# Optimization experiments

Measured on AMD Instinct MI355X. Metric: run time of the kernel, lower is better.

Reference implementation:

```python
import jax, jax.numpy as jnp
import numpy as np

N = 50000
E = 800000
D_IN, D_HID, D_OUT = 128, 128, 64
BN_EPS = 1e-5

def _glorot(key, shape):
    fan_in = shape[-1]
    return jax.random.normal(key, shape, dtype=jnp.float32) / jnp.sqrt(jnp.float32(fan_in))

def setup_inputs() -> dict:
    key = jax.random.key(0)
    ks = jax.random.split(key, 16)
    x = jax.random.normal(ks[0], (N, D_IN), dtype=jnp.float32)
    edge_index = jax.random.randint(ks[1], (2, E), 0, N, dtype=jnp.int64)
    edge_pairs = jax.random.randint(ks[2], (2, E), 0, N, dtype=jnp.int64)
    return {
        "x": x,
        "edge_index": edge_index,
        "edge_pairs": edge_pairs,
        # SAGEConv1: lin_l (bias) on aggregated neighbors, lin_r (no bias) on root
        "c1_Wl": _glorot(ks[3], (D_HID, D_IN)),
        "c1_bl": jnp.zeros((D_HID,), jnp.float32),
        "c1_Wr": _glorot(ks[4], (D_HID, D_IN)),
        # BatchNorm1d (eval mode: running stats)
        "bn_gamma": jnp.ones((D_HID,), jnp.float32),
        "bn_beta": jnp.zeros((D_HID,), jnp.float32),
        "bn_mean": jnp.zeros((D_HID,), jnp.float32),
        "bn_var": jnp.ones((D_HID,), jnp.float32),
        # SAGEConv2
        "c2_Wl": _glorot(ks[5], (D_OUT, D_HID)),
        "c2_bl": jnp.zeros((D_OUT,), jnp.float32),
        "c2_Wr": _glorot(ks[6], (D_OUT, D_HID)),
        # EdgeRegHead MLP: Linear(2*D_OUT, D_OUT) -> ReLU -> Linear(D_OUT, D_OUT//2) -> ReLU -> Linear(D_OUT//2, 1) -> Sigmoid
        "e_W1": _glorot(ks[7], (D_OUT, 2 * D_OUT)),
        "e_b1": jnp.zeros((D_OUT,), jnp.float32),
        "e_W2": _glorot(ks[8], (D_OUT // 2, D_OUT)),
        "e_b2": jnp.zeros((D_OUT // 2,), jnp.float32),
        "e_W3": _glorot(ks[9], (1, D_OUT // 2)),
        "e_b3": jnp.zeros((1,), jnp.float32),
    }

def _sage_conv(x, src, dst, Wl, bl, Wr):
    # mean-aggregate source features at destination nodes (PyG SAGEConv mean aggr)
    msg_sum = jax.ops.segment_sum(x[src], dst, num_segments=N)          # [N, d]
    cnt = jax.ops.segment_sum(jnp.ones((src.shape[0],), x.dtype), dst, num_segments=N)
    mean = msg_sum / jnp.maximum(cnt, 1.0)[:, None]
    return mean @ Wl.T + bl + x @ Wr.T

def reference(x, edge_index, edge_pairs,
              c1_Wl, c1_bl, c1_Wr,
              bn_gamma, bn_beta, bn_mean, bn_var,
              c2_Wl, c2_bl, c2_Wr,
              e_W1, e_b1, e_W2, e_b2, e_W3, e_b3):
    src, dst = edge_index[0], edge_index[1]
    h = _sage_conv(x, src, dst, c1_Wl, c1_bl, c1_Wr)                    # [N, D_HID]
    h = (h - bn_mean) * jax.lax.rsqrt(bn_var + BN_EPS) * bn_gamma + bn_beta
    h = jax.nn.relu(h)                                                   # dropout inactive (eval)
    z = _sage_conv(h, src, dst, c2_Wl, c2_bl, c2_Wr)                    # [N, D_OUT]
    zi = z[edge_pairs[0]]                                               # [P, D_OUT]
    zj = z[edge_pairs[1]]
    e = jnp.concatenate([zi, zj], axis=-1)                              # [P, 2*D_OUT]
    e = jax.nn.relu(e @ e_W1.T + e_b1)
    e = jax.nn.relu(e @ e_W2.T + e_b2)
    return jax.nn.sigmoid(e @ e_W3.T + e_b3)                            # [P, 1]
```

## Files before the change

### kernel.cpp

```cpp
#include <hip/hip_runtime.h>
#include <hip/hip_bf16.h>
#include <math.h>

#define NN 50000
#define NE 800000
#define DIN 128
#define DHID 128
#define DOUT 64
#define BN_EPS 1e-5f

typedef __attribute__((ext_vector_type(8))) short bf16x8;
typedef __attribute__((ext_vector_type(8))) _Float16 f16x8;
typedef __attribute__((ext_vector_type(4))) _Float16 f16x4;
typedef __attribute__((ext_vector_type(2))) _Float16 f16x2;
typedef __attribute__((ext_vector_type(4))) float f32x4;
typedef unsigned short ushort_t;
typedef unsigned int uint_t;

__device__ __forceinline__ ushort_t f2bf(float f) {
    uint_t u = __float_as_uint(f);
    uint_t r = (u + 0x7FFFu + ((u >> 16) & 1u)) >> 16;
    return (ushort_t)r;
}

__device__ __forceinline__ uint_t pk2bf(float a, float b) {
    __hip_bfloat16 x = __float2bfloat16(a);
    __hip_bfloat16 y = __float2bfloat16(b);
    ushort_t ux = *reinterpret_cast<ushort_t*>(&x);
    ushort_t uy = *reinterpret_cast<ushort_t*>(&y);
    return (uint_t)ux | ((uint_t)uy << 16);
}

__global__ __launch_bounds__(256) void k_deg_xcast(
    const int* __restrict__ ei, int* __restrict__ deg,
    const float* __restrict__ x, _Float16* __restrict__ xh)
{
    int b = blockIdx.x;
    if (b < 3125) {
        int e = b * 256 + threadIdx.x;
        atomicAdd(deg + ei[NE + e], 1);
    } else {
        int i = (b - 3125) * 256 + threadIdx.x;
        const float4* src = (const float4*)x + (size_t)i * 2;
        float4 a = src[0], c = src[1];
        f16x8 o;
        o[0] = (_Float16)a.x; o[1] = (_Float16)a.y; o[2] = (_Float16)a.z; o[3] = (_Float16)a.w;
        o[4] = (_Float16)c.x; o[5] = (_Float16)c.y; o[6] = (_Float16)c.z; o[7] = (_Float16)c.w;
        *(f16x8*)(xh + (size_t)i * 8) = o;
    }
}

__global__ __launch_bounds__(256) void k_scan1_prep(
    const int* __restrict__ deg, int* __restrict__ part,
    const float* __restrict__ c1_Wl, const float* __restrict__ c1_Wr,
    const float* __restrict__ c2_Wl, const float* __restrict__ c2_Wr,
    const float* __restrict__ gam, const float* __restrict__ bet,
    const float* __restrict__ bmean, const float* __restrict__ bvar,
    const float* __restrict__ eW1, const float* __restrict__ eW2,
    _Float16* __restrict__ w1cat, _Float16* __restrict__ w2cat,
    ushort_t* __restrict__ w1bf, ushort_t* __restrict__ w2bf,
    float* __restrict__ bnsc, float* __restrict__ bnsh)
{
    int t = threadIdx.x;
    if (blockIdx.x < 49) {
        __shared__ int s[256];
        int g = blockIdx.x * 256 + t;
        int v = 0;
        if (g < 12500) { int4 d = ((const int4*)deg)[g]; v = d.x + d.y + d.z + d.w; }
        s[t] = v;
        __syncthreads();
        #pragma unroll
        for (int off = 128; off > 0; off >>= 1) {
            if (t < off) s[t] += s[t + off];
            __syncthreads();
        }
        if (t == 0) part[blockIdx.x] = s[0];
    } else {
        for (int i = t; i < 128 * 128; i += 256) {
            int row = i >> 7, k = i & 127;
            w1cat[row * 256 + k]       = (_Float16)c1_Wl[i];
            w1cat[row * 256 + 128 + k] = (_Float16)c1_Wr[i];
        }
        for (int i = t; i < 64 * 128; i += 256) {
            int row = i >> 7, k = i & 127;
            w2cat[row * 256 + k]       = (_Float16)c2_Wl[i];
            w2cat[row * 256 + 128 + k] = (_Float16)c2_Wr[i];
        }
        for (int i = t; i < 64 * 128; i += 256) w1bf[i] = f2bf(eW1[i]);
        for (int i = t; i < 32 * 64; i += 256)  w2bf[i] = f2bf(eW2[i]);
        for (int i = t; i < 128; i += 256) {
            float s = gam[i] * rsqrtf(bvar[i] + BN_EPS);
            bnsc[i] = s;
            bnsh[i] = bet[i] - bmean[i] * s;
        }
    }
}

__global__ __launch_bounds__(256) void k_scan3(
    const int* __restrict__ deg, const int* __restrict__ part, int* __restrict__ rowptr)
{
    __shared__ int s[256];
    __shared__ int p[64];
    int t = threadIdx.x;
    int b = blockIdx.x;
    int g = b * 256 + t;
    int4 d = make_int4(0, 0, 0, 0);
    if (g < 12500) d = ((const int4*)deg)[g];
    int sum4 = d.x + d.y + d.z + d.w;
    s[t] = sum4;
    if (t < 49) p[t] = part[t];
    __syncthreads();
    #pragma unroll
    for (int off = 1; off < 256; off <<= 1) {
        int v = (t >= off) ? s[t - off] : 0;
        __syncthreads();
        s[t] += v;
        __syncthreads();
    }
    int blockoff = 0;
    for (int i = 0; i < b; ++i) blockoff += p[i];
    int off0 = blockoff + s[t] - sum4;
    if (g < 12500) {
        int4 o;
        o.x = off0;
        o.y = off0 + d.x;
        o.z = o.y + d.y;
        o.w = o.z + d.z;
        ((int4*)rowptr)[g] = o;
        if (g == 12499) rowptr[NN] = o.w + d.w;
    }
}

__global__ __launch_bounds__(256) void k_fill(
    const int* __restrict__ ei, const int* __restrict__ rowptr,
    int* __restrict__ cursor, int* __restrict__ csr_src)
{
    int e = blockIdx.x * blockDim.x + threadIdx.x;
    if (e >= NE) return;
    int dst = ei[NE + e];
    int slot = atomicAdd(cursor + dst, 1);
    csr_src[rowptr[dst] + slot] = ei[e];
}

#define GATHER4(feat)                                                          \
    {                                                                          \
        _Pragma("unroll 1")                                                    \
        for (int q = 0; q < 4; ++q) {                                          \
            int n = w * 4 + q;                                                 \
            int node = tile * 16 + n;                                          \
            int beg = __builtin_amdgcn_readfirstlane(rowptr[node]);            \
            int end = __builtin_amdgcn_readfirstlane(rowptr[node + 1]);        \
            float2 a0 = {0.f,0.f}, a1 = {0.f,0.f}, a2 = {0.f,0.f}, a3 = {0.f,0.f}; \
            float2 a4 = {0.f,0.f}, a5 = {0.f,0.f}, a6 = {0.f,0.f}, a7 = {0.f,0.f}; \
            int j = beg;                                                       \
            for (; j + 7 < end; j += 8) {                                      \
                int s0 = csr_src[j];     int s1 = csr_src[j + 1];              \
                int s2 = csr_src[j + 2]; int s3 = csr_src[j + 3];              \
                int s4 = csr_src[j + 4]; int s5 = csr_src[j + 5];              \
                int s6 = csr_src[j + 6]; int s7 = csr_src[j + 7];              \
                f16x2 v0 = *(const f16x2*)(feat + (size_t)s0 * 128 + lane * 2);\
                f16x2 v1 = *(const f16x2*)(feat + (size_t)s1 * 128 + lane * 2);\
                f16x2 v2 = *(const f16x2*)(feat + (size_t)s2 * 128 + lane * 2);\
                f16x2 v3 = *(const f16x2*)(feat + (size_t)s3 * 128 + lane * 2);\
                f16x2 v4 = *(const f16x2*)(feat + (size_t)s4 * 128 + lane * 2);\
                f16x2 v5 = *(const f16x2*)(feat + (size_t)s5 * 128 + lane * 2);\
                f16x2 v6 = *(const f16x2*)(feat + (size_t)s6 * 128 + lane * 2);\
                f16x2 v7 = *(const f16x2*)(feat + (size_t)s7 * 128 + lane * 2);\
                a0.x += (float)v0[0]; a0.y += (float)v0[1];                    \
                a1.x += (float)v1[0]; a1.y += (float)v1[1];                    \
                a2.x += (float)v2[0]; a2.y += (float)v2[1];                    \
                a3.x += (float)v3[0]; a3.y += (float)v3[1];                    \
                a4.x += (float)v4[0]; a4.y += (float)v4[1];                    \
                a5.x += (float)v5[0]; a5.y += (float)v5[1];                    \
                a6.x += (float)v6[0]; a6.y += (float)v6[1];                    \
                a7.x += (float)v7[0]; a7.y += (float)v7[1];                    \
            }                                                                  \
            for (; j + 1 < end; j += 2) {                                      \
                int s0 = csr_src[j];                                           \
                int s1 = csr_src[j + 1];                                       \
                f16x2 v0 = *(const f16x2*)(feat + (size_t)s0 * 128 + lane * 2);\
                f16x2 v1 = *(const f16x2*)(feat + (size_t)s1 * 128 + lane * 2);\
                a0.x += (float)v0[0]; a0.y += (float)v0[1];                    \
                a1.x += (float)v1[0]; a1.y += (float)v1[1];                    \
            }                                                                  \
            if (j < end) {                                                     \
                int s0 = csr_src[j];                                           \
                f16x2 v0 = *(const f16x2*)(feat + (size_t)s0 * 128 + lane * 2);\
                a0.x += (float)v0[0]; a0.y += (float)v0[1];                    \
            }                                                                  \
            float inv = 1.0f / fmaxf((float)(end - beg), 1.0f);                \
            f16x2 o;                                                           \
            o[0] = (_Float16)((a0.x + a1.x + a2.x + a3.x + a4.x + a5.x + a6.x + a7.x) * inv); \
            o[1] = (_Float16)((a0.y + a1.y + a2.y + a3.y + a4.y + a5.y + a6.y + a7.y) * inv); \
            uint_t off = (uint_t)(n * 256 + lane * 4) ^ (uint_t)((n & 7) << 4);\
            *(f16x2*)((char*)mlds + off) = o;                                  \
        }                                                                      \
    }

__global__ __launch_bounds__(256) void k_gconv1(
    const _Float16* __restrict__ xh, const int* __restrict__ rowptr,
    const int* __restrict__ csr_src,
    const _Float16* __restrict__ w1cat, const float* __restrict__ bl,
    const float* __restrict__ bnsc, const float* __restrict__ bnsh,
    _Float16* __restrict__ hh)
{
    __shared__ _Float16 mlds[16 * 128];
    const int tid = threadIdx.x;
    const int lane = tid & 63;
    const int w = tid >> 6;
    const int tile = blockIdx.x;
    const int e = lane & 15;
    const int c = lane >> 4;
    const int node = tile * 16 + e;

    f16x8 wf[2][8];
    #pragma unroll
    for (int nt = 0; nt < 2; ++nt)
        #pragma unroll
        for (int ks = 0; ks < 8; ++ks)
            wf[nt][ks] = *(const f16x8*)(w1cat + (size_t)(w * 32 + nt * 16 + e) * 256 + ks * 32 + c * 8);
    f16x8 bfx[4];
    #pragma unroll
    for (int ks = 0; ks < 4; ++ks)
        bfx[ks] = *(const f16x8*)(xh + (size_t)node * 128 + ks * 32 + c * 8);
    f32x4 acc[2];
    #pragma unroll
    for (int nt = 0; nt < 2; ++nt)
        acc[nt] = *(const f32x4*)(bl + w * 32 + nt * 16 + c * 4);

    GATHER4(xh);
    __syncthreads();

    f16x8 bfm[4];
    #pragma unroll
    for (int ks = 0; ks < 4; ++ks) {
        uint_t off = (uint_t)(e * 256 + ks * 64 + c * 16) ^ (uint_t)((e & 7) << 4);
        bfm[ks] = *(const f16x8*)((const char*)mlds + off);
    }

    #pragma unroll
    for (int ks = 0; ks < 4; ++ks)
        #pragma unroll
        for (int nt = 0; nt < 2; ++nt)
            acc[nt] = __builtin_amdgcn_mfma_f32_16x16x32_f16(wf[nt][ks], bfm[ks], acc[nt], 0, 0, 0);
    #pragma unroll
    for (int ks = 0; ks < 4; ++ks)
        #pragma unroll
        for (int nt = 0; nt < 2; ++nt)
            acc[nt] = __builtin_amdgcn_mfma_f32_16x16x32_f16(wf[nt][ks + 4], bfx[ks], acc[nt], 0, 0, 0);

    #pragma unroll
    for (int nt = 0; nt < 2; ++nt) {
        int j0 = w * 32 + nt * 16 + c * 4;
        f32x4 sc = *(const f32x4*)(bnsc + j0);
        f32x4 sh = *(const f32x4*)(bnsh + j0);
        f16x4 o;
        #pragma unroll
        for (int r = 0; r < 4; ++r)
            o[r] = (_Float16)fmaxf(acc[nt][r] * sc[r] + sh[r], 0.f);
        *(f16x4*)(hh + (size_t)node * 128 + j0) = o;
    }
}

__global__ __launch_bounds__(256) void k_gconv2(
    const _Float16* __restrict__ hh, const int* __restrict__ rowptr,
    const int* __restrict__ csr_src,
    const _Float16* __restrict__ w2cat, const float* __restrict__ bl,
    ushort_t* __restrict__ zbf)
{
    __shared__ _Float16 mlds[16 * 128];
    const int tid = threadIdx.x;
    const int lane = tid & 63;
    const int w = tid >> 6;
    const int tile = blockIdx.x;
    const int e = lane & 15;
    const int c = lane >> 4;
    const int node = tile * 16 + e;

    f16x8 wf[8];
    #pragma unroll
    for (int ks = 0; ks < 8; ++ks)
        wf[ks] = *(const f16x8*)(w2cat + (size_t)(w * 16 + e) * 256 + ks * 32 + c * 8);
    f16x8 bfx[4];
    #pragma unroll
    for (int ks = 0; ks < 4; ++ks)
        bfx[ks] = *(const f16x8*)(hh + (size_t)node * 128 + ks * 32 + c * 8);
    f32x4 acc = *(const f32x4*)(bl + w * 16 + c * 4);

    GATHER4(hh);
    __syncthreads();

    f16x8 bfm[4];
    #pragma unroll
    for (int ks = 0; ks < 4; ++ks) {
        uint_t off = (uint_t)(e * 256 + ks * 64 + c * 16) ^ (uint_t)((e & 7) << 4);
        bfm[ks] = *(const f16x8*)((const char*)mlds + off);
    }

    #pragma unroll
    for (int ks = 0; ks < 4; ++ks)
        acc = __builtin_amdgcn_mfma_f32_16x16x32_f16(wf[ks], bfm[ks], acc, 0, 0, 0);
    #pragma unroll
    for (int ks = 0; ks < 4; ++ks)
        acc = __builtin_amdgcn_mfma_f32_16x16x32_f16(wf[ks + 4], bfx[ks], acc, 0, 0, 0);

    int j0 = w * 16 + c * 4;
    uint2 pk;
    pk.x = pk2bf(acc[0], acc[1]);
    pk.y = pk2bf(acc[2], acc[3]);
    *(uint2*)(zbf + (size_t)node * 64 + j0) = pk;
}

__global__ __launch_bounds__(256) void k_edge(
    const ushort_t* __restrict__ zbf, const int* __restrict__ ep,
    const ushort_t* __restrict__ w1bf, const float* __restrict__ b1,
    const ushort_t* __restrict__ w2bf, const float* __restrict__ b2,
    const float* __restrict__ W3, const float* __restrict__ b3,
    float* __restrict__ out)
{
    __shared__ ushort_t a1lds[4][16 * 64];
    const int tid  = threadIdx.x;
    const int lane = tid & 63;
    const int e    = lane & 15;
    const int c    = lane >> 4;
    ushort_t* lds  = &a1lds[tid >> 6][0];
    const uint_t swz = (uint_t)((e & 7) << 4);

    bf16x8 w1f[4][4];
    #pragma unroll
    for (int mt = 0; mt < 4; ++mt)
        #pragma unroll
        for (int ks = 0; ks < 4; ++ks)
            w1f[mt][ks] = *(const bf16x8*)(w1bf + (mt * 16 + e) * 128 + ks * 32 + c * 8);

    bf16x8 w2f[2][2];
    #pragma unroll
    for (int mt2 = 0; mt2 < 2; ++mt2)
        #pragma unroll
        for (int ks2 = 0; ks2 < 2; ++ks2)
            w2f[mt2][ks2] = *(const bf16x8*)(w2bf + (mt2 * 16 + e) * 64 + ks2 * 32 + c * 8);

    f32x4 bias1[4];
    #pragma unroll
    for (int mt = 0; mt < 4; ++mt) bias1[mt] = *(const f32x4*)(b1 + mt * 16 + c * 4);
    f32x4 bias2[2];
    #pragma unroll
    for (int mt2 = 0; mt2 < 2; ++mt2) bias2[mt2] = *(const f32x4*)(b2 + mt2 * 16 + c * 4);
    f32x4 w3v[2];
    #pragma unroll
    for (int mt2 = 0; mt2 < 2; ++mt2) w3v[mt2] = *(const f32x4*)(W3 + mt2 * 16 + c * 4);
    const float b3v = b3[0];

    const int nw = (gridDim.x * blockDim.x) >> 6;
    const int NT = NE / 16;

#define LOADZ(T, dst)                                                         \
    {                                                                         \
        int p = (T) * 16 + e;                                                 \
        int ni = ep[p];                                                       \
        int nj = ep[NE + p];                                                  \
        const ushort_t* zi = zbf + (size_t)ni * DOUT;                         \
        const ushort_t* zj = zbf + (size_t)nj * DOUT;                         \
        dst[0] = *(const bf16x8*)(zi + c * 8);                                \
        dst[1] = *(const bf16x8*)(zi + 32 + c * 8);                           \
        dst[2] = *(const bf16x8*)(zj + c * 8);                                \
        dst[3] = *(const bf16x8*)(zj + 32 + c * 8);                           \
    }

#define COMPUTE(T, bfr)                                                       \
    {                                                                         \
        f32x4 acc[4];                                                         \
        _Pragma("unroll")                                                     \
        for (int mt = 0; mt < 4; ++mt) acc[mt] = bias1[mt];                   \
        __builtin_amdgcn_s_setprio(1);                                        \
        _Pragma("unroll")                                                     \
        for (int ks = 0; ks < 4; ++ks)                                        \
            _Pragma("unroll")                                                 \
            for (int mt = 0; mt < 4; ++mt)                                    \
                acc[mt] = __builtin_amdgcn_mfma_f32_16x16x32_bf16(            \
                    w1f[mt][ks], bfr[ks], acc[mt], 0, 0, 0);                  \
        __builtin_amdgcn_s_setprio(0);                                        \
        _Pragma("unroll")                                                     \
        for (int mt = 0; mt < 4; ++mt) {                                      \
            uint_t lo = pk2bf(fmaxf(acc[mt][0], 0.f), fmaxf(acc[mt][1], 0.f));\
            uint_t hi = pk2bf(fmaxf(acc[mt][2], 0.f), fmaxf(acc[mt][3], 0.f));\
            uint_t off = (uint_t)(e * 128 + mt * 32 + c * 8) ^ swz;           \
            *(uint2*)((char*)lds + off) = make_uint2(lo, hi);                 \
        }                                                                     \
        bf16x8 b2f[2];                                                        \
        _Pragma("unroll")                                                     \
        for (int ks2 = 0; ks2 < 2; ++ks2) {                                   \
            uint_t off = (uint_t)(e * 128 + ks2 * 64 + c * 16) ^ swz;         \
            b2f[ks2] = *(const bf16x8*)((const char*)lds + off);              \
        }                                                                     \
        f32x4 a2[2];                                                          \
        _Pragma("unroll")                                                     \
        for (int mt2 = 0; mt2 < 2; ++mt2) a2[mt2] = bias2[mt2];               \
        __builtin_amdgcn_s_setprio(1);                                        \
        _Pragma("unroll")                                                     \
        for (int ks2 = 0; ks2 < 2; ++ks2)                                     \
            _Pragma("unroll")                                                 \
            for (int mt2 = 0; mt2 < 2; ++mt2)                                 \
                a2[mt2] = __builtin_amdgcn_mfma_f32_16x16x32_bf16(            \
                    w2f[mt2][ks2], b2f[ks2], a2[mt2], 0, 0, 0);               \
        __builtin_amdgcn_s_setprio(0);                                        \
        float t3 = b3v;                                                       \
        _Pragma("unroll")                                                     \
        for (int mt2 = 0; mt2 < 2; ++mt2)                                     \
            _Pragma("unroll")                                                 \
            for (int r = 0; r < 4; ++r)                                       \
                t3 += fmaxf(a2[mt2][r], 0.f) * w3v[mt2][r];                   \
        t3 += __shfl_xor(t3, 16);                                             \
        t3 += __shfl_xor(t3, 32);                                             \
        if (lane < 16) {                                                      \
            float ex = __expf(-t3);                                           \
            out[(T) * 16 + lane] = __builtin_amdgcn_rcpf(1.f + ex);           \
        }                                                                     \
    }

    bf16x8 zA[4], zB[4];
    int tile = (blockIdx.x * blockDim.x + tid) >> 6;
    if (tile >= NT) return;
    LOADZ(tile, zA);
    while (tile < NT) {
        int nx = tile + nw;
        if (nx < NT) LOADZ(nx, zB);
        COMPUTE(tile, zA);
        tile = nx;
        if (tile >= NT) break;
        nx = tile + nw;
        if (nx < NT) LOADZ(nx, zA);
        COMPUTE(tile, zB);
        tile = nx;
    }

#undef LOADZ
#undef COMPUTE
}

extern "C" void kernel_launch(void* const* d_in, const int* in_sizes, int n_in,
                              void* d_out, int out_size, void* d_ws, size_t ws_size,
                              hipStream_t stream)
{
    const float* x     = (const float*)d_in[0];
    const int*   ei    = (const int*)d_in[1];
    const int*   ep    = (const int*)d_in[2];
    const float* c1_Wl = (const float*)d_in[3];
    const float* c1_bl = (const float*)d_in[4];
    const float* c1_Wr = (const float*)d_in[5];
    const float* bn_g  = (const float*)d_in[6];
    const float* bn_b  = (const float*)d_in[7];
    const float* bn_m  = (const float*)d_in[8];
    const float* bn_v  = (const float*)d_in[9];
    const float* c2_Wl = (const float*)d_in[10];
    const float* c2_bl = (const float*)d_in[11];
    const float* c2_Wr = (const float*)d_in[12];
    const float* e_W1  = (const float*)d_in[13];
    const float* e_b1  = (const float*)d_in[14];
    const float* e_W2  = (const float*)d_in[15];
    const float* e_b2  = (const float*)d_in[16];
    const float* e_W3  = (const float*)d_in[17];
    const float* e_b3  = (const float*)d_in[18];
    float* out = (float*)d_out;

    _Float16* xh    = (_Float16*)d_ws;
    _Float16* meanh = xh + (size_t)NN * DIN;
    _Float16* hh    = meanh + (size_t)NN * DIN;
    ushort_t* zbf   = (ushort_t*)(hh + (size_t)NN * DHID);
    _Float16* w1cat = (_Float16*)(zbf + (size_t)NN * DOUT);
    _Float16* w2cat = w1cat + 128 * 256;
    ushort_t* w1bf  = (ushort_t*)(w2cat + 64 * 256);
    ushort_t* w2bf  = w1bf + 64 * 128;
    float*    bnsc  = (float*)(w2bf + 32 * 64);
    float*    bnsh  = bnsc + 128;
    int*      deg     = (int*)(bnsh + 128);
    int*      cursor  = deg + 50048;
    int*      rowptr  = cursor + 50048;
    int*      csr_src = rowptr + 50052;
    int*      part    = csr_src + 800000;

    hipMemsetAsync(deg, 0, (size_t)(50048 * 2) * sizeof(int), stream);

    k_deg_xcast<<<6250, 256, 0, stream>>>(ei, deg, x, xh);
    k_scan1_prep<<<50, 256, 0, stream>>>(deg, part,
                                         c1_Wl, c1_Wr, c2_Wl, c2_Wr,
                                         bn_g, bn_b, bn_m, bn_v, e_W1, e_W2,
                                         w1cat, w2cat, w1bf, w2bf, bnsc, bnsh);
    k_scan3<<<49, 256, 0, stream>>>(deg, part, rowptr);
    k_fill <<<3125, 256, 0, stream>>>(ei, rowptr, cursor, csr_src);

    k_gconv1<<<3125, 256, 0, stream>>>(xh, rowptr, csr_src, w1cat, c1_bl, bnsc, bnsh, hh);
    k_gconv2<<<3125, 256, 0, stream>>>(hh, rowptr, csr_src, w2cat, c2_bl, zbf);

    k_edge<<<1280, 256, 0, stream>>>(zbf, ep, w1bf, e_b1, w2bf, e_b2,
                                     e_W3, e_b3, out);
}
```

Baseline: 295.7 us.

## Project layer-2 features before aggregation to halve gather width

Adds a kernel that computes h·Wl^T (64-wide fp16) per node before aggregation, so the second conv gathers 64-wide projected rows instead of 128-wide hidden rows and then adds the mean to the root-term MFMA result. This uses linearity of mean aggregation to cut the gather traffic of layer 2 in half, at the cost of an extra kernel launch and an extra pass over hh. Also removes s_setprio hints in the edge MLP and changes the edge kernel grid size. Gathers are now per-lane scalar fp16 loads, which may be less efficient per byte.

```diff
diff --git a/kernel.cpp b/kernel.cpp
--- a/kernel.cpp
+++ b/kernel.cpp
@@ -142,14 +142,14 @@
     csr_src[rowptr[dst] + slot] = ei[e];
 }
 
-#define GATHER4(feat)                                                          \
+#define GATHER4_128(feat)                                                      \
     {                                                                          \
         _Pragma("unroll 1")                                                    \
         for (int q = 0; q < 4; ++q) {                                          \
             int n = w * 4 + q;                                                 \
-            int node = tile * 16 + n;                                          \
-            int beg = __builtin_amdgcn_readfirstlane(rowptr[node]);            \
-            int end = __builtin_amdgcn_readfirstlane(rowptr[node + 1]);        \
+            int node4 = tile * 16 + n;                                         \
+            int beg = __builtin_amdgcn_readfirstlane(rowptr[node4]);           \
+            int end = __builtin_amdgcn_readfirstlane(rowptr[node4 + 1]);       \
             float2 a0 = {0.f,0.f}, a1 = {0.f,0.f}, a2 = {0.f,0.f}, a3 = {0.f,0.f}; \
             float2 a4 = {0.f,0.f}, a5 = {0.f,0.f}, a6 = {0.f,0.f}, a7 = {0.f,0.f}; \
             int j = beg;                                                       \
@@ -228,7 +228,7 @@
     for (int nt = 0; nt < 2; ++nt)
         acc[nt] = *(const f32x4*)(bl + w * 32 + nt * 16 + c * 4);
 
-    GATHER4(xh);
+    GATHER4_128(xh);
     __syncthreads();
 
     f16x8 bfm[4];
@@ -262,13 +262,44 @@
     }
 }
 
+__global__ __launch_bounds__(256) void k_hw(
+    const _Float16* __restrict__ hh, const _Float16* __restrict__ w2cat,
+    _Float16* __restrict__ hw)
+{
+    const int tid = threadIdx.x;
+    const int lane = tid & 63;
+    const int e = lane & 15;
+    const int c = lane >> 4;
+    const int w = tid >> 6;
+    const int node = blockIdx.x * 16 + e;
+
+    f16x8 wf[4];
+    #pragma unroll
+    for (int ks = 0; ks < 4; ++ks)
+        wf[ks] = *(const f16x8*)(w2cat + (size_t)(w * 16 + e) * 256 + ks * 32 + c * 8);
+    f16x8 bf[4];
+    #pragma unroll
+    for (int ks = 0; ks < 4; ++ks)
+        bf[ks] = *(const f16x8*)(hh + (size_t)node * 128 + ks * 32 + c * 8);
+
+    f32x4 acc = {0.f, 0.f, 0.f, 0.f};
+    #pragma unroll
+    for (int ks = 0; ks < 4; ++ks)
+        acc = __builtin_amdgcn_mfma_f32_16x16x32_f16(wf[ks], bf[ks], acc, 0, 0, 0);
+
+    f16x4 o;
+    #pragma unroll
+    for (int r = 0; r < 4; ++r) o[r] = (_Float16)acc[r];
+    *(f16x4*)(hw + (size_t)node * 64 + w * 16 + c * 4) = o;
+}
+
 __global__ __launch_bounds__(256) void k_gconv2(
-    const _Float16* __restrict__ hh, const int* __restrict__ rowptr,
-    const int* __restrict__ csr_src,
+    const _Float16* __restrict__ hh, const _Float16* __restrict__ hw,
+    const int* __restrict__ rowptr, const int* __restrict__ csr_src,
     const _Float16* __restrict__ w2cat, const float* __restrict__ bl,
     ushort_t* __restrict__ zbf)
 {
-    __shared__ _Float16 mlds[16 * 128];
+    __shared__ float mlds32[16 * 64];
     const int tid = threadIdx.x;
     const int lane = tid & 63;
     const int w = tid >> 6;
@@ -277,32 +308,65 @@
     const int c = lane >> 4;
     const int node = tile * 16 + e;
 
-    f16x8 wf[8];
-    #pragma unroll
-    for (int ks = 0; ks < 8; ++ks)
-        wf[ks] = *(const f16x8*)(w2cat + (size_t)(w * 16 + e) * 256 + ks * 32 + c * 8);
+    f16x8 wf[4];
+    #pragma unroll
+    for (int ks = 0; ks < 4; ++ks)
+        wf[ks] = *(const f16x8*)(w2cat + (size_t)(w * 16 + e) * 256 + 128 + ks * 32 + c * 8);
     f16x8 bfx[4];
     #pragma unroll
     for (int ks = 0; ks < 4; ++ks)
         bfx[ks] = *(const f16x8*)(hh + (size_t)node * 128 + ks * 32 + c * 8);
+
+    #pragma unroll 1
+    for (int q = 0; q < 4; ++q) {
+        int n = w * 4 + q;
+        int node4 = tile * 16 + n;
+        int beg = __builtin_amdgcn_readfirstlane(rowptr[node4]);
+        int end = __builtin_amdgcn_readfirstlane(rowptr[node4 + 1]);
+        float a0 = 0.f, a1 = 0.f, a2 = 0.f, a3 = 0.f;
+        float a4 = 0.f, a5 = 0.f, a6 = 0.f, a7 = 0.f;
+        int j = beg;
+        for (; j + 7 < end; j += 8) {
+            int s0 = csr_src[j];     int s1 = csr_src[j + 1];
+            int s2 = csr_src[j + 2]; int s3 = csr_src[j + 3];
+            int s4 = csr_src[j + 4]; int s5 = csr_src[j + 5];
+            int s6 = csr_src[j + 6]; int s7 = csr_src[j + 7];
+            a0 += (float)hw[(size_t)s0 * 64 + lane];
+            a1 += (float)hw[(size_t)s1 * 64 + lane];
+            a2 += (float)hw[(size_t)s2 * 64 + lane];
+            a3 += (float)hw[(size_t)s3 * 64 + lane];
+            a4 += (float)hw[(size_t)s4 * 64 + lane];
+            a5 += (float)hw[(size_t)s5 * 64 + lane];
+            a6 += (float)hw[(size_t)s6 * 64 + lane];
+            a7 += (float)hw[(size_t)s7 * 64 + lane];
+        }
+        for (; j + 1 < end; j += 2) {
+            int s0 = csr_src[j];
+            int s1 = csr_src[j + 1];
+            a0 += (float)hw[(size_t)s0 * 64 + lane];
+            a1 += (float)hw[(size_t)s1 * 64 + lane];
+        }
+        if (j < end) {
+            int s0 = csr_src[j];
+            a0 += (float)hw[(size_t)s0 * 64 + lane];
+        }
+        float inv = 1.0f / fmaxf((float)(end - beg), 1.0f);
+        float m = (a0 + a1 + a2 + a3 + a4 + a5 + a6 + a7) * inv;
+        uint_t off = (uint_t)(n * 256 + lane * 4) ^ (uint_t)((n & 7) << 4);
+        *(float*)((char*)mlds32 + off) = m;
+    }
+    __syncthreads();
+
     f32x4 acc = *(const f32x4*)(bl + w * 16 + c * 4);
-
-    GATHER4(hh);
-    __syncthreads();
-
-    f16x8 bfm[4];
-    #pragma unroll
-    for (int ks = 0; ks < 4; ++ks) {
-        uint_t off = (uint_t)(e * 256 + ks * 64 + c * 16) ^ (uint_t)((e & 7) << 4);
-        bfm[ks] = *(const f16x8*)((const char*)mlds + off);
-    }
-
-    #pragma unroll
-    for (int ks = 0; ks < 4; ++ks)
-        acc = __builtin_amdgcn_mfma_f32_16x16x32_f16(wf[ks], bfm[ks], acc, 0, 0, 0);
-    #pragma unroll
-    for (int ks = 0; ks < 4; ++ks)
-        acc = __builtin_amdgcn_mfma_f32_16x16x32_f16(wf[ks + 4], bfx[ks], acc, 0, 0, 0);
+    {
+        uint_t off = (uint_t)(e * 256 + (w * 16 + c * 4) * 4) ^ (uint_t)((e & 7) << 4);
+        f32x4 mv = *(const f32x4*)((const char*)mlds32 + off);
+        acc[0] += mv[0]; acc[1] += mv[1]; acc[2] += mv[2]; acc[3] += mv[3];
+    }
+
+    #pragma unroll
+    for (int ks = 0; ks < 4; ++ks)
+        acc = __builtin_amdgcn_mfma_f32_16x16x32_f16(wf[ks], bfx[ks], acc, 0, 0, 0);
 
     int j0 = w * 16 + c * 4;
     uint2 pk;
@@ -372,14 +436,12 @@
         f32x4 acc[4];                                                         \
         _Pragma("unroll")                                                     \
         for (int mt = 0; mt < 4; ++mt) acc[mt] = bias1[mt];                   \
-        __builtin_amdgcn_s_setprio(1);                                        \
         _Pragma("unroll")                                                     \
         for (int ks = 0; ks < 4; ++ks)                                        \
             _Pragma("unroll")                                                 \
             for (int mt = 0; mt < 4; ++mt)                                    \
                 acc[mt] = __builtin_amdgcn_mfma_f32_16x16x32_bf16(            \
                     w1f[mt][ks], bfr[ks], acc[mt], 0, 0, 0);                  \
-        __builtin_amdgcn_s_setprio(0);                                        \
         _Pragma("unroll")                                                     \
         for (int mt = 0; mt < 4; ++mt) {                                      \
             uint_t lo = pk2bf(fmaxf(acc[mt][0], 0.f), fmaxf(acc[mt][1], 0.f));\
@@ -396,14 +458,12 @@
         f32x4 a2[2];                                                          \
         _Pragma("unroll")                                                     \
         for (int mt2 = 0; mt2 < 2; ++mt2) a2[mt2] = bias2[mt2];               \
-        __builtin_amdgcn_s_setprio(1);                                        \
         _Pragma("unroll")                                                     \
         for (int ks2 = 0; ks2 < 2; ++ks2)                                     \
             _Pragma("unroll")                                                 \
             for (int mt2 = 0; mt2 < 2; ++mt2)                                 \
                 a2[mt2] = __builtin_amdgcn_mfma_f32_16x16x32_bf16(            \
                     w2f[mt2][ks2], b2f[ks2], a2[mt2], 0, 0, 0);               \
-        __builtin_amdgcn_s_setprio(0);                                        \
         float t3 = b3v;                                                       \
         _Pragma("unroll")                                                     \
         for (int mt2 = 0; mt2 < 2; ++mt2)                                     \
@@ -464,8 +524,8 @@
     float* out = (float*)d_out;
 
     _Float16* xh    = (_Float16*)d_ws;
-    _Float16* meanh = xh + (size_t)NN * DIN;
-    _Float16* hh    = meanh + (size_t)NN * DIN;
+    _Float16* hwbuf = xh + (size_t)NN * DIN;
+    _Float16* hh    = hwbuf + (size_t)NN * DIN;
     ushort_t* zbf   = (ushort_t*)(hh + (size_t)NN * DHID);
     _Float16* w1cat = (_Float16*)(zbf + (size_t)NN * DOUT);
     _Float16* w2cat = w1cat + 128 * 256;
@@ -490,8 +550,9 @@
     k_fill <<<3125, 256, 0, stream>>>(ei, rowptr, cursor, csr_src);
 
     k_gconv1<<<3125, 256, 0, stream>>>(xh, rowptr, csr_src, w1cat, c1_bl, bnsc, bnsh, hh);
-    k_gconv2<<<3125, 256, 0, stream>>>(hh, rowptr, csr_src, w2cat, c2_bl, zbf);
-
-    k_edge<<<1280, 256, 0, stream>>>(zbf, ep, w1bf, e_b1, w2bf, e_b2,
+    k_hw    <<<3125, 256, 0, stream>>>(hh, w2cat, hwbuf);
+    k_gconv2<<<3125, 256, 0, stream>>>(hh, hwbuf, rowptr, csr_src, w2cat, c2_bl, zbf);
+
+    k_edge<<<1024, 256, 0, stream>>>(zbf, ep, w1bf, e_b1, w2bf, e_b2,
                                      e_W3, e_b3, out);
 }
```

After: 284.0 us. 1.04x faster.
